# Kernel tuning notes

Measured on AMD Instinct MI355X. Metric: run time of the kernel, lower is better.

Reference implementation:

```python
import jax, jax.numpy as jnp
import numpy as np
from jax import lax

EPS = 1e-08


def setup_inputs() -> dict:
    key = jax.random.key(0)
    kX, kY, kXs, kW, kA, kB1, kB2 = jax.random.split(key, 7)
    P, D, K, M = 8192, 1024, 131072, 512
    return {
        "X": jax.random.normal(kX, (P, D), dtype=jnp.float32),
        "y": jax.random.normal(kY, (P,), dtype=jnp.float32),
        "X_star": jax.random.normal(kXs, (K, D), dtype=jnp.float32),
        "gamma": jnp.float32(0.001),
        "W": jax.random.normal(kW, (M, D), dtype=jnp.float32) * 0.01,
        "a": jax.random.normal(kA, (M,), dtype=jnp.float32) * 0.01,
        "b1": jax.random.normal(kB1, (M,), dtype=jnp.float32) * 0.01,
        "b2": jnp.float32(0.1),
        "L": 64,
    }


def reference(X, y, X_star, gamma, W, a, b1, b2, L):
    P, D = X.shape
    Sigma_hat = (X.T @ X) / P                      # (D, D)
    I = jnp.eye(D, dtype=X.dtype)
    M_mat = I - (gamma / L) * Sigma_hat            # (D, D)

    # S = sum_{l=0}^{L-1} M^l, built sequentially as in the original loop
    def step(carry, _):
        S, Mp = carry
        return (S + Mp, Mp @ M_mat), None

    (S, _), _ = lax.scan(step, (jnp.zeros_like(I), I), None, length=L)

    rep = gamma * (S @ (X.T @ y))                  # (D,)
    linear_pred = (X_star @ rep) / (L * P)         # (K,)

    rep_normalized = rep / (jnp.linalg.norm(rep) + EPS)
    phi = X_star * rep_normalized                  # (K, D) elementwise
    hidden = jax.nn.relu(phi @ W.T + b1)           # (K, m)
    mlp_correction = hidden @ a                    # (K,)
    return linear_pred + mlp_correction + b2
```

## Files before the change

kernel.cpp:

```cpp
#include <hip/hip_runtime.h>
#include <hip/hip_bf16.h>
#include <stdint.h>

#define D_DIM 1024
#define P_ROWS 8192
#define K_ROWS 131072
#define M_DIM 512
#define L_STEPS 64
#define BM 128
#define LDP 40

typedef short bf16x8_t __attribute__((ext_vector_type(8)));
typedef float f32x4_t __attribute__((ext_vector_type(4)));

__device__ __forceinline__ uint32_t f2bf(float f) {
  union { float f; uint32_t u; } c; c.f = f;
  const uint32_t u = c.u;
  return (u + 0x7FFFu + ((u >> 16) & 1u)) >> 16;
}
__device__ __forceinline__ uint32_t pack2(float lo, float hi) {
  return f2bf(lo) | (f2bf(hi) << 16);
}

__global__ void xty_kernel(const float* __restrict__ X, const float* __restrict__ y,
                           float* __restrict__ v) {
  const int d0 = threadIdx.x * 4;
  float a0 = 0.f, a1 = 0.f, a2 = 0.f, a3 = 0.f;
  for (int i = blockIdx.x; i < P_ROWS; i += gridDim.x) {
    const float s = y[i];
    const float4 x = *reinterpret_cast<const float4*>(X + (size_t)i * D_DIM + d0);
    a0 += s * x.x; a1 += s * x.y; a2 += s * x.z; a3 += s * x.w;
  }
  atomicAdd(v + d0 + 0, a0);
  atomicAdd(v + d0 + 1, a1);
  atomicAdd(v + d0 + 2, a2);
  atomicAdd(v + d0 + 3, a3);
}

__global__ void xtxw_kernel(const float* __restrict__ X, const float* __restrict__ win,
                            float* __restrict__ wout) {
  __shared__ float red[4][D_DIM];
  const int lane = threadIdx.x & 63;
  const int wave = threadIdx.x >> 6;
  const int gw = blockIdx.x * 4 + wave;
  const int nw = gridDim.x * 4;
  float wv[16], acc[16];
#pragma unroll
  for (int q = 0; q < 4; ++q) {
    const float4 tv = *reinterpret_cast<const float4*>(win + q * 256 + lane * 4);
    wv[q*4+0] = tv.x; wv[q*4+1] = tv.y; wv[q*4+2] = tv.z; wv[q*4+3] = tv.w;
  }
#pragma unroll
  for (int j = 0; j < 16; ++j) acc[j] = 0.f;
  for (int i = gw; i < P_ROWS; i += nw) {
    const float* xr = X + (size_t)i * D_DIM;
    float xv[16];
    float dot = 0.f;
#pragma unroll
    for (int q = 0; q < 4; ++q) {
      const float4 tv = *reinterpret_cast<const float4*>(xr + q * 256 + lane * 4);
      xv[q*4+0] = tv.x; xv[q*4+1] = tv.y; xv[q*4+2] = tv.z; xv[q*4+3] = tv.w;
      dot += tv.x * wv[q*4+0] + tv.y * wv[q*4+1] + tv.z * wv[q*4+2] + tv.w * wv[q*4+3];
    }
#pragma unroll
    for (int m = 1; m < 64; m <<= 1) dot += __shfl_xor(dot, m);
#pragma unroll
    for (int j = 0; j < 16; ++j) acc[j] += dot * xv[j];
  }
#pragma unroll
  for (int q = 0; q < 4; ++q) {
    float4 tv;
    tv.x = acc[q*4+0]; tv.y = acc[q*4+1]; tv.z = acc[q*4+2]; tv.w = acc[q*4+3];
    *reinterpret_cast<float4*>(&red[wave][q * 256 + lane * 4]) = tv;
  }
  __syncthreads();
  const int d0 = threadIdx.x * 4;
#pragma unroll
  for (int j = 0; j < 4; ++j)
    atomicAdd(wout + d0 + j, red[0][d0+j] + red[1][d0+j] + red[2][d0+j] + red[3][d0+j]);
}

__global__ void combine_kernel(const float* __restrict__ v, const float* __restrict__ u1,
                               const float* __restrict__ u2, const float* __restrict__ gamma_p,
                               float* __restrict__ rep_lin, float* __restrict__ repn) {
  __shared__ float sred[4];
  const float gamma = *gamma_p;
  const float eps = gamma / (float)L_STEPS;
  const float c1 = 2016.0f * eps / (float)P_ROWS;
  const float c2 = 41664.0f * eps * eps / ((float)P_ROWS * (float)P_ROWS);
  const int d0 = threadIdx.x * 4;
  float r[4];
  float ss = 0.f;
#pragma unroll
  for (int j = 0; j < 4; ++j) {
    const float val = gamma * ((float)L_STEPS * v[d0+j] - c1 * u1[d0+j] + c2 * u2[d0+j]);
    r[j] = val;
    ss += val * val;
  }
#pragma unroll
  for (int m = 1; m < 64; m <<= 1) ss += __shfl_xor(ss, m);
  if ((threadIdx.x & 63) == 0) sred[threadIdx.x >> 6] = ss;
  __syncthreads();
  const float norm = sqrtf(sred[0] + sred[1] + sred[2] + sred[3]);
  const float inv_norm = 1.0f / (norm + 1e-8f);
  const float lin_s = 1.0f / ((float)L_STEPS * (float)P_ROWS);
#pragma unroll
  for (int j = 0; j < 4; ++j) {
    rep_lin[d0+j] = r[j] * lin_s;
    repn[d0+j]    = r[j] * inv_norm;
  }
}

__global__ void wn_kernel(const float* __restrict__ W, const float* __restrict__ repn,
                          ushort* __restrict__ Wn) {
  const int m = blockIdx.x;
  const int d0 = threadIdx.x * 4;
  const float4 w  = *reinterpret_cast<const float4*>(W + (size_t)m * D_DIM + d0);
  const float4 rn = *reinterpret_cast<const float4*>(repn + d0);
  ushort4 o;
  o.x = (ushort)f2bf(w.x * rn.x);
  o.y = (ushort)f2bf(w.y * rn.y);
  o.z = (ushort)f2bf(w.z * rn.z);
  o.w = (ushort)f2bf(w.w * rn.w);
  *reinterpret_cast<ushort4*>(Wn + (size_t)m * D_DIM + d0) = o;
}

__global__ __launch_bounds__(512, 2)
void fused_kernel(const float* __restrict__ Xs, const ushort* __restrict__ Wn,
                  const float* __restrict__ rep_lin, const float* __restrict__ b1,
                  const float* __restrict__ aw, const float* __restrict__ b2p,
                  float* __restrict__ out) {
  __shared__ ushort Alds[2][BM * LDP];
  __shared__ ushort Blds[2][M_DIM * LDP];
  __shared__ float mlp_acc[BM];
  __shared__ float lin_acc[BM];

  const int t = threadIdx.x;
  const int lane = t & 63;
  const int wid = t >> 6;
  const int wm = wid >> 2;
  const int wn = wid & 3;
  const size_t blockRow = (size_t)blockIdx.x * BM;

  if (t < BM) mlp_acc[t] = 0.f;

  const int arow = t >> 2;
  const int kchunk = (t & 3) * 8;

  const float*  Arow = Xs + (blockRow + (size_t)arow) * D_DIM + kchunk;
  const ushort* Brow = Wn + (size_t)arow * D_DIM + kchunk;

  float linreg = 0.f;

  {
    const float4 a0 = *reinterpret_cast<const float4*>(Arow);
    const float4 a1 = *reinterpret_cast<const float4*>(Arow + 4);
    const uint4 b0 = *reinterpret_cast<const uint4*>(Brow + 0 * 128 * D_DIM);
    const uint4 b1q = *reinterpret_cast<const uint4*>(Brow + 1 * 128 * D_DIM);
    const uint4 b2q = *reinterpret_cast<const uint4*>(Brow + 2 * 128 * D_DIM);
    const uint4 b3q = *reinterpret_cast<const uint4*>(Brow + 3 * 128 * D_DIM);
    const float4 r0 = *reinterpret_cast<const float4*>(rep_lin + kchunk);
    const float4 r1 = *reinterpret_cast<const float4*>(rep_lin + kchunk + 4);
    linreg += a0.x*r0.x + a0.y*r0.y + a0.z*r0.z + a0.w*r0.w
            + a1.x*r1.x + a1.y*r1.y + a1.z*r1.z + a1.w*r1.w;
    uint4 ap;
    ap.x = pack2(a0.x, a0.y); ap.y = pack2(a0.z, a0.w);
    ap.z = pack2(a1.x, a1.y); ap.w = pack2(a1.z, a1.w);
    *reinterpret_cast<uint4*>(&Alds[0][arow * LDP + kchunk]) = ap;
    *reinterpret_cast<uint4*>(&Blds[0][(arow +   0) * LDP + kchunk]) = b0;
    *reinterpret_cast<uint4*>(&Blds[0][(arow + 128) * LDP + kchunk]) = b1q;
    *reinterpret_cast<uint4*>(&Blds[0][(arow + 256) * LDP + kchunk]) = b2q;
    *reinterpret_cast<uint4*>(&Blds[0][(arow + 384) * LDP + kchunk]) = b3q;
  }

  f32x4_t acc[4][8];
#pragma unroll
  for (int mi = 0; mi < 4; ++mi)
#pragma unroll
    for (int ni = 0; ni < 8; ++ni)
      acc[mi][ni] = f32x4_t{0.f, 0.f, 0.f, 0.f};

  __syncthreads();

  const int fr = lane & 15;
  const int kg = lane >> 4;
  const int aoff = (wm * 64 + fr) * LDP + kg * 8;
  const int boff = (wn * 128 + fr) * LDP + kg * 8;

  for (int s = 0; s < 32; ++s) {
    const int cur = s & 1;
    float4 na0, na1; uint4 nb0, nb1, nb2, nb3;
    if (s < 31) {
      const float*  An = Arow + (s + 1) * 32;
      const ushort* Bn = Brow + (s + 1) * 32;
      na0 = *reinterpret_cast<const float4*>(An);
      na1 = *reinterpret_cast<const float4*>(An + 4);
      nb0 = *reinterpret_cast<const uint4*>(Bn + 0 * 128 * D_DIM);
      nb1 = *reinterpret_cast<const uint4*>(Bn + 1 * 128 * D_DIM);
      nb2 = *reinterpret_cast<const uint4*>(Bn + 2 * 128 * D_DIM);
      nb3 = *reinterpret_cast<const uint4*>(Bn + 3 * 128 * D_DIM);
    }
    const ushort* Ab = &Alds[cur][0];
    const ushort* Bb = &Blds[cur][0];
    bf16x8_t afr[4], bfr[8];
#pragma unroll
    for (int mi = 0; mi < 4; ++mi)
      afr[mi] = *reinterpret_cast<const bf16x8_t*>(Ab + aoff + mi * 16 * LDP);
#pragma unroll
    for (int ni = 0; ni < 8; ++ni)
      bfr[ni] = *reinterpret_cast<const bf16x8_t*>(Bb + boff + ni * 16 * LDP);
#pragma unroll
    for (int mi = 0; mi < 4; ++mi)
#pragma unroll
      for (int ni = 0; ni < 8; ++ni)
        acc[mi][ni] = __builtin_amdgcn_mfma_f32_16x16x32_bf16(afr[mi], bfr[ni], acc[mi][ni], 0, 0, 0);
    if (s < 31) {
      const int nxt = cur ^ 1;
      const float* rl = rep_lin + (s + 1) * 32 + kchunk;
      const float4 r0 = *reinterpret_cast<const float4*>(rl);
      const float4 r1 = *reinterpret_cast<const float4*>(rl + 4);
      linreg += na0.x*r0.x + na0.y*r0.y + na0.z*r0.z + na0.w*r0.w
              + na1.x*r1.x + na1.y*r1.y + na1.z*r1.z + na1.w*r1.w;
      uint4 ap;
      ap.x = pack2(na0.x, na0.y); ap.y = pack2(na0.z, na0.w);
      ap.z = pack2(na1.x, na1.y); ap.w = pack2(na1.z, na1.w);
      *reinterpret_cast<uint4*>(&Alds[nxt][arow * LDP + kchunk]) = ap;
      *reinterpret_cast<uint4*>(&Blds[nxt][(arow +   0) * LDP + kchunk]) = nb0;
      *reinterpret_cast<uint4*>(&Blds[nxt][(arow + 128) * LDP + kchunk]) = nb1;
      *reinterpret_cast<uint4*>(&Blds[nxt][(arow + 256) * LDP + kchunk]) = nb2;
      *reinterpret_cast<uint4*>(&Blds[nxt][(arow + 384) * LDP + kchunk]) = nb3;
    }
    __syncthreads();
  }

  linreg += __shfl_xor(linreg, 1);
  linreg += __shfl_xor(linreg, 2);
  if ((t & 3) == 0) lin_acc[arow] = linreg;

  float b1r[8], ar[8];
#pragma unroll
  for (int ni = 0; ni < 8; ++ni) {
    const int c = wn * 128 + ni * 16 + fr;
    b1r[ni] = b1[c];
    ar[ni]  = aw[c];
  }
#pragma unroll
  for (int mi = 0; mi < 4; ++mi) {
#pragma unroll
    for (int r = 0; r < 4; ++r) {
      float sum = 0.f;
#pragma unroll
      for (int ni = 0; ni < 8; ++ni) {
        const float h = acc[mi][ni][r] + b1r[ni];
        sum += fmaxf(h, 0.f) * ar[ni];
      }
      sum += __shfl_xor(sum, 1);
      sum += __shfl_xor(sum, 2);
      sum += __shfl_xor(sum, 4);
      sum += __shfl_xor(sum, 8);
      if (fr == 0) {
        const int row = wm * 64 + mi * 16 + kg * 4 + r;
        atomicAdd(&mlp_acc[row], sum);
      }
    }
  }
  __syncthreads();
  if (t < BM)
    out[blockRow + t] = lin_acc[t] + mlp_acc[t] + b2p[0];
}

extern "C" void kernel_launch(void* const* d_in, const int* in_sizes, int n_in,
                              void* d_out, int out_size, void* d_ws, size_t ws_size,
                              hipStream_t stream) {
  const float* X     = (const float*)d_in[0];
  const float* y     = (const float*)d_in[1];
  const float* Xs    = (const float*)d_in[2];
  const float* gamma = (const float*)d_in[3];
  const float* W     = (const float*)d_in[4];
  const float* a     = (const float*)d_in[5];
  const float* b1    = (const float*)d_in[6];
  const float* b2    = (const float*)d_in[7];
  float* out = (float*)d_out;

  char* ws = (char*)d_ws;
  float*  v       = (float*)(ws + 0);
  float*  u1      = (float*)(ws + 4096);
  float*  u2      = (float*)(ws + 8192);
  float*  rep_lin = (float*)(ws + 12288);
  float*  repn    = (float*)(ws + 16384);
  ushort* Wn      = (ushort*)(ws + 20480);

  hipMemsetAsync(ws, 0, 3 * 4096, stream);
  hipLaunchKernelGGL(xty_kernel,    dim3(128), dim3(256), 0, stream, X, y, v);
  hipLaunchKernelGGL(xtxw_kernel,   dim3(128), dim3(256), 0, stream, X, v, u1);
  hipLaunchKernelGGL(xtxw_kernel,   dim3(128), dim3(256), 0, stream, X, u1, u2);
  hipLaunchKernelGGL(combine_kernel, dim3(1),  dim3(256), 0, stream, v, u1, u2, gamma, rep_lin, repn);
  hipLaunchKernelGGL(wn_kernel,     dim3(M_DIM), dim3(256), 0, stream, W, repn, Wn);
  hipLaunchKernelGGL(fused_kernel,  dim3(K_ROWS / BM), dim3(512), 0, stream,
                     Xs, Wn, rep_lin, b1, a, b2, out);
}
```

Before: 364.4 us.

## Stream operands via direct global-to-LDS loads with pre-fragmented W and swizzled fp32 A

The W*repn product is now written in MFMA fragment order, so the main kernel can copy B tiles straight into LDS with global_load_lds and read them with conflict-free linear reads. X_star tiles are loaded as fp32 directly into a triple-buffered, XOR-swizzled LDS buffer and converted to bf16 at fragment-read time with v_cvt_pk_bf16_f32. The linear term reads from LDS and rep_lin is cached in shared memory. The aim is to drop the register round trip and VALU packing on the load path and overlap loads with MFMA using explicit waitcnt and barriers, at the cost of much more LDS per block (about 114KB), which may cut occupancy. The preprocessing kernels' grid sizes are also doubled.

```diff
diff --git a/kernel.cpp b/kernel.cpp
--- a/kernel.cpp
+++ b/kernel.cpp
@@ -8,18 +8,17 @@
 #define M_DIM 512
 #define L_STEPS 64
 #define BM 128
-#define LDP 40
 
 typedef short bf16x8_t __attribute__((ext_vector_type(8)));
 typedef float f32x4_t __attribute__((ext_vector_type(4)));
+
+typedef const __attribute__((address_space(1))) void* gas_t;
+typedef __attribute__((address_space(3))) void* las_t;
 
 __device__ __forceinline__ uint32_t f2bf(float f) {
   union { float f; uint32_t u; } c; c.f = f;
   const uint32_t u = c.u;
   return (u + 0x7FFFu + ((u >> 16) & 1u)) >> 16;
-}
-__device__ __forceinline__ uint32_t pack2(float lo, float hi) {
-  return f2bf(lo) | (f2bf(hi) << 16);
 }
 
 __global__ void xty_kernel(const float* __restrict__ X, const float* __restrict__ y,
@@ -111,67 +110,62 @@
   }
 }
 
-__global__ void wn_kernel(const float* __restrict__ W, const float* __restrict__ repn,
-                          ushort* __restrict__ Wn) {
-  const int m = blockIdx.x;
-  const int d0 = threadIdx.x * 4;
-  const float4 w  = *reinterpret_cast<const float4*>(W + (size_t)m * D_DIM + d0);
-  const float4 rn = *reinterpret_cast<const float4*>(repn + d0);
-  ushort4 o;
-  o.x = (ushort)f2bf(w.x * rn.x);
-  o.y = (ushort)f2bf(w.y * rn.y);
-  o.z = (ushort)f2bf(w.z * rn.z);
-  o.w = (ushort)f2bf(w.w * rn.w);
-  *reinterpret_cast<ushort4*>(Wn + (size_t)m * D_DIM + d0) = o;
+__global__ void wn_frag_kernel(const float* __restrict__ W, const float* __restrict__ repn,
+                               ushort* __restrict__ WnF) {
+  const int gid = blockIdx.x * 256 + threadIdx.x;
+  const int l = gid & 63;
+  const int f = (gid >> 6) & 31;
+  const int s = gid >> 11;
+  const int m = f * 16 + (l & 15);
+  const int d0 = s * 32 + ((l >> 4) << 3);
+  const float4 w0 = *reinterpret_cast<const float4*>(W + (size_t)m * D_DIM + d0);
+  const float4 w1 = *reinterpret_cast<const float4*>(W + (size_t)m * D_DIM + d0 + 4);
+  const float4 r0 = *reinterpret_cast<const float4*>(repn + d0);
+  const float4 r1 = *reinterpret_cast<const float4*>(repn + d0 + 4);
+  uint32_t p0 = f2bf(w0.x*r0.x) | (f2bf(w0.y*r0.y) << 16);
+  uint32_t p1 = f2bf(w0.z*r0.z) | (f2bf(w0.w*r0.w) << 16);
+  uint32_t p2 = f2bf(w1.x*r1.x) | (f2bf(w1.y*r1.y) << 16);
+  uint32_t p3 = f2bf(w1.z*r1.z) | (f2bf(w1.w*r1.w) << 16);
+  uint4 o; o.x = p0; o.y = p1; o.z = p2; o.w = p3;
+  *reinterpret_cast<uint4*>(WnF + (size_t)gid * 8) = o;
 }
 
 __global__ __launch_bounds__(512, 2)
-void fused_kernel(const float* __restrict__ Xs, const ushort* __restrict__ Wn,
+void fused_kernel(const float* __restrict__ Xs, const ushort* __restrict__ WnF,
                   const float* __restrict__ rep_lin, const float* __restrict__ b1,
                   const float* __restrict__ aw, const float* __restrict__ b2p,
                   float* __restrict__ out) {
-  __shared__ ushort Alds[2][BM * LDP];
-  __shared__ ushort Blds[2][M_DIM * LDP];
-  __shared__ float mlp_acc[BM];
-  __shared__ float lin_acc[BM];
+  __shared__ float  Af[3 * 4096];
+  __shared__ ushort Bh[2 * 16384];
+  __shared__ float  repl[D_DIM];
+  __shared__ float  mlp_acc[BM];
+  __shared__ float  lin_acc[BM];
 
   const int t = threadIdx.x;
   const int lane = t & 63;
   const int wid = t >> 6;
   const int wm = wid >> 2;
   const int wn = wid & 3;
+  const int fr = lane & 15;
+  const int kg = lane >> 4;
   const size_t blockRow = (size_t)blockIdx.x * BM;
 
-  if (t < BM) mlp_acc[t] = 0.f;
-
-  const int arow = t >> 2;
-  const int kchunk = (t & 3) * 8;
-
-  const float*  Arow = Xs + (blockRow + (size_t)arow) * D_DIM + kchunk;
-  const ushort* Brow = Wn + (size_t)arow * D_DIM + kchunk;
-
-  float linreg = 0.f;
-
-  {
-    const float4 a0 = *reinterpret_cast<const float4*>(Arow);
-    const float4 a1 = *reinterpret_cast<const float4*>(Arow + 4);
-    const uint4 b0 = *reinterpret_cast<const uint4*>(Brow + 0 * 128 * D_DIM);
-    const uint4 b1q = *reinterpret_cast<const uint4*>(Brow + 1 * 128 * D_DIM);
-    const uint4 b2q = *reinterpret_cast<const uint4*>(Brow + 2 * 128 * D_DIM);
-    const uint4 b3q = *reinterpret_cast<const uint4*>(Brow + 3 * 128 * D_DIM);
-    const float4 r0 = *reinterpret_cast<const float4*>(rep_lin + kchunk);
-    const float4 r1 = *reinterpret_cast<const float4*>(rep_lin + kchunk + 4);
-    linreg += a0.x*r0.x + a0.y*r0.y + a0.z*r0.z + a0.w*r0.w
-            + a1.x*r1.x + a1.y*r1.y + a1.z*r1.z + a1.w*r1.w;
-    uint4 ap;
-    ap.x = pack2(a0.x, a0.y); ap.y = pack2(a0.z, a0.w);
-    ap.z = pack2(a1.x, a1.y); ap.w = pack2(a1.z, a1.w);
-    *reinterpret_cast<uint4*>(&Alds[0][arow * LDP + kchunk]) = ap;
-    *reinterpret_cast<uint4*>(&Blds[0][(arow +   0) * LDP + kchunk]) = b0;
-    *reinterpret_cast<uint4*>(&Blds[0][(arow + 128) * LDP + kchunk]) = b1q;
-    *reinterpret_cast<uint4*>(&Blds[0][(arow + 256) * LDP + kchunk]) = b2q;
-    *reinterpret_cast<uint4*>(&Blds[0][(arow + 384) * LDP + kchunk]) = b3q;
-  }
+  char* AfB = (char*)Af;
+  char* BhB = (char*)Bh;
+  const char* WnB = (const char*)WnF;
+  const char* replB = (const char*)repl;
+
+  const char* gA0 = (const char*)Xs
+      + (blockRow + (size_t)wid * 16 + (lane >> 3)) * (D_DIM * 4)
+      + (size_t)(((lane & 7) ^ (lane >> 3)) * 16);
+  const char* gA1 = gA0 + (size_t)8 * (D_DIM * 4);
+
+  const int aoff0 = (wm * 64 + fr) * 128 + (((kg * 2)     ^ (lane & 7)) * 16);
+  const int aoff1 = (wm * 64 + fr) * 128 + (((kg * 2 + 1) ^ (lane & 7)) * 16);
+  const int rowL = t >> 2;
+  const int cL = (t & 3) * 2;
+  const int loffA0 = rowL * 128 + ((cL      ^ (rowL & 7)) * 16);
+  const int loffA1 = rowL * 128 + (((cL | 1) ^ (rowL & 7)) * 16);
 
   f32x4_t acc[4][8];
 #pragma unroll
@@ -179,63 +173,83 @@
 #pragma unroll
     for (int ni = 0; ni < 8; ++ni)
       acc[mi][ni] = f32x4_t{0.f, 0.f, 0.f, 0.f};
-
-  __syncthreads();
-
-  const int fr = lane & 15;
-  const int kg = lane >> 4;
-  const int aoff = (wm * 64 + fr) * LDP + kg * 8;
-  const int boff = (wn * 128 + fr) * LDP + kg * 8;
-
-  for (int s = 0; s < 32; ++s) {
-    const int cur = s & 1;
-    float4 na0, na1; uint4 nb0, nb1, nb2, nb3;
-    if (s < 31) {
-      const float*  An = Arow + (s + 1) * 32;
-      const ushort* Bn = Brow + (s + 1) * 32;
-      na0 = *reinterpret_cast<const float4*>(An);
-      na1 = *reinterpret_cast<const float4*>(An + 4);
-      nb0 = *reinterpret_cast<const uint4*>(Bn + 0 * 128 * D_DIM);
-      nb1 = *reinterpret_cast<const uint4*>(Bn + 1 * 128 * D_DIM);
-      nb2 = *reinterpret_cast<const uint4*>(Bn + 2 * 128 * D_DIM);
-      nb3 = *reinterpret_cast<const uint4*>(Bn + 3 * 128 * D_DIM);
+  float linreg = 0.f;
+
+  auto stageB = [&](int sn) {
+    const char* src = WnB + (size_t)sn * 32768 + (size_t)wid * 4096 + (size_t)lane * 16;
+    char* dst = BhB + (size_t)(sn & 1) * 32768 + (size_t)wid * 4096;
+#pragma unroll
+    for (int j = 0; j < 4; ++j)
+      __builtin_amdgcn_global_load_lds((gas_t)(src + j * 1024), (las_t)(dst + j * 1024), 16, 0, 0);
+  };
+  auto stageA = [&](int s2) {
+    char* dst = AfB + (size_t)(s2 % 3) * 16384 + (size_t)wid * 2048;
+    __builtin_amdgcn_global_load_lds((gas_t)(gA0 + (size_t)s2 * 128), (las_t)dst, 16, 0, 0);
+    __builtin_amdgcn_global_load_lds((gas_t)(gA1 + (size_t)s2 * 128), (las_t)(dst + 1024), 16, 0, 0);
+  };
+  auto compute = [&](int s) {
+    const char* Ab = AfB + (size_t)(s % 3) * 16384;
+    const char* Bb = BhB + (size_t)(s & 1) * 32768;
+    bf16x8_t bfr[8];
+#pragma unroll
+    for (int ni = 0; ni < 8; ++ni)
+      bfr[ni] = *reinterpret_cast<const bf16x8_t*>(Bb + wn * 8192 + ni * 1024 + lane * 16);
+    bf16x8_t afr[4];
+#pragma unroll
+    for (int mi = 0; mi < 4; ++mi) {
+      f32x4_t v0 = *reinterpret_cast<const f32x4_t*>(Ab + aoff0 + mi * 2048);
+      f32x4_t v1 = *reinterpret_cast<const f32x4_t*>(Ab + aoff1 + mi * 2048);
+      uint32_t p0, p1, p2, p3;
+      asm("v_cvt_pk_bf16_f32 %0, %1, %2" : "=v"(p0) : "v"(v0[0]), "v"(v0[1]));
+      asm("v_cvt_pk_bf16_f32 %0, %1, %2" : "=v"(p1) : "v"(v0[2]), "v"(v0[3]));
+      asm("v_cvt_pk_bf16_f32 %0, %1, %2" : "=v"(p2) : "v"(v1[0]), "v"(v1[1]));
+      asm("v_cvt_pk_bf16_f32 %0, %1, %2" : "=v"(p3) : "v"(v1[2]), "v"(v1[3]));
+      union { uint32_t u[4]; bf16x8_t h; } cv;
+      cv.u[0] = p0; cv.u[1] = p1; cv.u[2] = p2; cv.u[3] = p3;
+      afr[mi] = cv.h;
     }
-    const ushort* Ab = &Alds[cur][0];
-    const ushort* Bb = &Blds[cur][0];
-    bf16x8_t afr[4], bfr[8];
-#pragma unroll
-    for (int mi = 0; mi < 4; ++mi)
-      afr[mi] = *reinterpret_cast<const bf16x8_t*>(Ab + aoff + mi * 16 * LDP);
-#pragma unroll
-    for (int ni = 0; ni < 8; ++ni)
-      bfr[ni] = *reinterpret_cast<const bf16x8_t*>(Bb + boff + ni * 16 * LDP);
 #pragma unroll
     for (int mi = 0; mi < 4; ++mi)
 #pragma unroll
       for (int ni = 0; ni < 8; ++ni)
         acc[mi][ni] = __builtin_amdgcn_mfma_f32_16x16x32_bf16(afr[mi], bfr[ni], acc[mi][ni], 0, 0, 0);
-    if (s < 31) {
-      const int nxt = cur ^ 1;
-      const float* rl = rep_lin + (s + 1) * 32 + kchunk;
-      const float4 r0 = *reinterpret_cast<const float4*>(rl);
-      const float4 r1 = *reinterpret_cast<const float4*>(rl + 4);
-      linreg += na0.x*r0.x + na0.y*r0.y + na0.z*r0.z + na0.w*r0.w
-              + na1.x*r1.x + na1.y*r1.y + na1.z*r1.z + na1.w*r1.w;
-      uint4 ap;
-      ap.x = pack2(na0.x, na0.y); ap.y = pack2(na0.z, na0.w);
-      ap.z = pack2(na1.x, na1.y); ap.w = pack2(na1.z, na1.w);
-      *reinterpret_cast<uint4*>(&Alds[nxt][arow * LDP + kchunk]) = ap;
-      *reinterpret_cast<uint4*>(&Blds[nxt][(arow +   0) * LDP + kchunk]) = nb0;
-      *reinterpret_cast<uint4*>(&Blds[nxt][(arow + 128) * LDP + kchunk]) = nb1;
-      *reinterpret_cast<uint4*>(&Blds[nxt][(arow + 256) * LDP + kchunk]) = nb2;
-      *reinterpret_cast<uint4*>(&Blds[nxt][(arow + 384) * LDP + kchunk]) = nb3;
-    }
-    __syncthreads();
-  }
+    f32x4_t la0 = *reinterpret_cast<const f32x4_t*>(Ab + loffA0);
+    f32x4_t la1 = *reinterpret_cast<const f32x4_t*>(Ab + loffA1);
+    f32x4_t lr0 = *reinterpret_cast<const f32x4_t*>(replB + s * 128 + (t & 3) * 32);
+    f32x4_t lr1 = *reinterpret_cast<const f32x4_t*>(replB + s * 128 + (t & 3) * 32 + 16);
+    linreg += la0[0]*lr0[0] + la0[1]*lr0[1] + la0[2]*lr0[2] + la0[3]*lr0[3]
+            + la1[0]*lr1[0] + la1[1]*lr1[1] + la1[2]*lr1[2] + la1[3]*lr1[3];
+  };
+
+  stageB(0);
+  stageA(0);
+  stageA(1);
+  if (t < BM) mlp_acc[t] = 0.f;
+  repl[t] = rep_lin[t];
+  repl[t + 512] = rep_lin[t + 512];
+  asm volatile("s_waitcnt vmcnt(0)" ::: "memory");
+  __syncthreads();
+
+  for (int s = 0; s < 30; ++s) {
+    stageB(s + 1);
+    stageA(s + 2);
+    __builtin_amdgcn_sched_barrier(0);
+    compute(s);
+    asm volatile("s_waitcnt vmcnt(2)" ::: "memory");
+    __builtin_amdgcn_sched_barrier(0);
+    __builtin_amdgcn_s_barrier();
+  }
+  stageB(31);
+  __builtin_amdgcn_sched_barrier(0);
+  compute(30);
+  asm volatile("s_waitcnt vmcnt(0)" ::: "memory");
+  __builtin_amdgcn_sched_barrier(0);
+  __builtin_amdgcn_s_barrier();
+  compute(31);
 
   linreg += __shfl_xor(linreg, 1);
   linreg += __shfl_xor(linreg, 2);
-  if ((t & 3) == 0) lin_acc[arow] = linreg;
+  if ((t & 3) == 0) lin_acc[rowL] = linreg;
 
   float b1r[8], ar[8];
 #pragma unroll
@@ -288,14 +302,14 @@
   float*  u2      = (float*)(ws + 8192);
   float*  rep_lin = (float*)(ws + 12288);
   float*  repn    = (float*)(ws + 16384);
-  ushort* Wn      = (ushort*)(ws + 20480);
+  ushort* WnF     = (ushort*)(ws + 20480);
 
   hipMemsetAsync(ws, 0, 3 * 4096, stream);
-  hipLaunchKernelGGL(xty_kernel,    dim3(128), dim3(256), 0, stream, X, y, v);
-  hipLaunchKernelGGL(xtxw_kernel,   dim3(128), dim3(256), 0, stream, X, v, u1);
-  hipLaunchKernelGGL(xtxw_kernel,   dim3(128), dim3(256), 0, stream, X, u1, u2);
-  hipLaunchKernelGGL(combine_kernel, dim3(1),  dim3(256), 0, stream, v, u1, u2, gamma, rep_lin, repn);
-  hipLaunchKernelGGL(wn_kernel,     dim3(M_DIM), dim3(256), 0, stream, W, repn, Wn);
-  hipLaunchKernelGGL(fused_kernel,  dim3(K_ROWS / BM), dim3(512), 0, stream,
-                     Xs, Wn, rep_lin, b1, a, b2, out);
-}
+  hipLaunchKernelGGL(xty_kernel,     dim3(256), dim3(256), 0, stream, X, y, v);
+  hipLaunchKernelGGL(xtxw_kernel,    dim3(256), dim3(256), 0, stream, X, v, u1);
+  hipLaunchKernelGGL(xtxw_kernel,    dim3(256), dim3(256), 0, stream, X, u1, u2);
+  hipLaunchKernelGGL(combine_kernel, dim3(1),   dim3(256), 0, stream, v, u1, u2, gamma, rep_lin, repn);
+  hipLaunchKernelGGL(wn_frag_kernel, dim3(256), dim3(256), 0, stream, W, repn, WnF);
+  hipLaunchKernelGGL(fused_kernel,   dim3(K_ROWS / BM), dim3(512), 0, stream,
+                     Xs, WnF, rep_lin, b1, a, b2, out);
+}
```

Measured after the change: 342.6 us. 1.06x faster.
